# Kernel optimization log

Measured on AMD Instinct MI355X. Metric: run time of the kernel, lower is better.

Reference implementation:

```python
import jax, jax.numpy as jnp
import numpy as np

PATCH = 3  # patch_size=3 -> 3x3 displacement window, kernel_size=1, stride=1, dilation_patch=1

def _corr_level(feat1, feat2, channels):
    # spatial_correlation_sample(feat1, feat2, kernel_size=1, patch_size=3,
    #                            stride=1, padding=0, dilation_patch=1)
    # out[b, pi, pj, y, x] = sum_c feat1[b,c,y,x] * feat2[b,c, y+pi-1, x+pj-1]
    b, c, h, w = feat1.shape
    f2p = jnp.pad(feat2, ((0, 0), (0, 0), (1, 1), (1, 1)))  # zero pad displacements
    planes = []
    for di in range(PATCH):
        for dj in range(PATCH):
            planes.append(jnp.sum(feat1 * f2p[:, :, di:di + h, dj:dj + w], axis=1))
    corr = jnp.stack(planes, axis=1)  # [b, 9, h, w] == view(b, ph*pw, h, w)
    return jax.nn.leaky_relu(corr / channels, negative_slope=0.01)


def setup_inputs() -> dict:
    key = jax.random.key(0)
    chans = [512, 1024, 512, 256, 256, 256]
    sizes = [64, 32, 16, 8, 4, 2]
    B = 16
    ks = jax.random.split(key, 12)
    inp = {}
    for i, (c, s) in enumerate(zip(chans, sizes)):
        inp[f"x_pre{i}"] = jax.random.normal(ks[i], (B, c, s, s), dtype=jnp.float32)
        inp[f"x{i}"] = jax.random.normal(ks[6 + i], (B, c, s, s), dtype=jnp.float32)
    return inp


def reference(x_pre0, x_pre1, x_pre2, x_pre3, x_pre4, x_pre5,
              x0, x1, x2, x3, x4, x5):
    chans = [512, 1024, 512, 256, 256, 256]
    x_pre = [x_pre0, x_pre1, x_pre2, x_pre3, x_pre4, x_pre5]
    x = [x0, x1, x2, x3, x4, x5]
    # zip(x, x_pre): feat1 comes from x (current), feat2 from x_pre (previous)
    return tuple(_corr_level(f1, f2, c) for f1, f2, c in zip(x, x_pre, chans))
```

## Files before the change

kernel.cpp:

```cpp
#include <hip/hip_runtime.h>
#include <stdint.h>


struct Lv {
  const float* f1;
  const float* f2;
  float* dst;
  int C, ss, csize;
  uint32_t tiles;
  uint32_t npix;
  uint32_t blk_end;
};
struct P { Lv lv[6]; };

struct Fv {
  const float* src;
  uint32_t end;
  uint32_t cstride;
  uint32_t nchunk;
  int ss;
  float invC;
};
struct PF { Fv f[6]; uint32_t total; };

#define LOADIT(A, R0, R1, R2)                 \
  do {                                        \
    (A) = *(const float2*)f1p;                \
    (R0) = *(const float2*)(f2b + ro0);       \
    (R1) = *(const float2*)(f2b + ro1);       \
    (R2) = *(const float2*)(f2b + ro2);       \
    f1p += S2;                                \
    f2b += S2;                                \
  } while (0)

#define FMAROW(A, R, r)                                   \
  do {                                                    \
    const float pw = __shfl_up((R).y, 1);                 \
    const float nx = __shfl_down((R).x, 1);               \
    acc[r][0][0] = fmaf((A).x, pw, acc[r][0][0]);         \
    acc[r][0][1] = fmaf((A).y, (R).x, acc[r][0][1]);      \
    acc[r][1][0] = fmaf((A).x, (R).x, acc[r][1][0]);      \
    acc[r][1][1] = fmaf((A).y, (R).y, acc[r][1][1]);      \
    acc[r][2][0] = fmaf((A).x, (R).y, acc[r][2][0]);      \
    acc[r][2][1] = fmaf((A).y, nx, acc[r][2][1]);         \
  } while (0)

#define FMAIT(A, R0, R1, R2) \
  do {                       \
    FMAROW(A, R0, 0);        \
    FMAROW(A, R1, 1);        \
    FMAROW(A, R2, 2);        \
  } while (0)

__global__ __launch_bounds__(512, 6) void corr_part(P p) {
  __shared__ float red[8][9 * 128];

  const uint32_t bid = blockIdx.x;
  int l = 0;
#pragma unroll
  for (int i = 0; i < 5; ++i) l += (bid >= p.lv[i].blk_end) ? 1 : 0;
  const Lv L = p.lv[l];
  const uint32_t local = bid - (l ? p.lv[l - 1].blk_end : 0u);
  const uint32_t chunk = local / L.tiles;
  const uint32_t tile = local - chunk * L.tiles;

  const int w = (int)(threadIdx.x >> 6);
  const int lane = (int)(threadIdx.x & 63u);
  const int ss = L.ss;
  const int S = 1 << ss;
  const int S2 = 1 << (2 * ss);

  uint32_t pix0 = tile * 128u + ((uint32_t)lane << 1);
  if (pix0 >= L.npix) pix0 = L.npix - 2u;
  const uint32_t b = pix0 >> (2 * ss);
  const uint32_t yx = pix0 & (uint32_t)(S2 - 1);
  const int y = (int)(yx >> ss);
  const int x0 = (int)(yx & (uint32_t)(S - 1));
  (void)x0;

  const uint32_t c0 = chunk * (uint32_t)(8 * L.csize) + (uint32_t)(w * L.csize);
  const size_t pbase = ((size_t)(b * (uint32_t)L.C + c0)) << (2 * ss);
  const float* __restrict__ f1p = L.f1 + pbase + yx;
  const float* __restrict__ f2b = L.f2 + pbase;

  int yy0 = y - 1;
  yy0 = yy0 < 0 ? 0 : yy0;
  int yy2 = y + 1;
  yy2 = yy2 > S - 1 ? S - 1 : yy2;
  const int xb = (int)(yx & (uint32_t)(S - 1));
  const int ro0 = yy0 * S + xb;
  const int ro1 = y * S + xb;
  const int ro2 = yy2 * S + xb;

  float acc[3][3][2];
#pragma unroll
  for (int r = 0; r < 3; ++r)
#pragma unroll
    for (int d = 0; d < 3; ++d)
#pragma unroll
      for (int e = 0; e < 2; ++e) acc[r][d][e] = 0.f;

  const int n = L.csize;
  float2 a0, u0, v0, w0;
  float2 a1, u1, v1, w1;
  LOADIT(a0, u0, v0, w0);
#pragma unroll 1
  for (int j = 0; j + 2 < n; j += 2) {
    LOADIT(a1, u1, v1, w1);
    FMAIT(a0, u0, v0, w0);
    LOADIT(a0, u0, v0, w0);
    FMAIT(a1, u1, v1, w1);
  }
  LOADIT(a1, u1, v1, w1);
  FMAIT(a0, u0, v0, w0);
  FMAIT(a1, u1, v1, w1);

#pragma unroll
  for (int r = 0; r < 3; ++r)
#pragma unroll
    for (int d = 0; d < 3; ++d) {
      const int t = r * 3 + d;
      *(float2*)&red[w][t * 128 + lane * 2] = make_float2(acc[r][d][0], acc[r][d][1]);
    }

  __syncthreads();

  float* dbase = L.dst + (size_t)chunk * 9u * (size_t)L.npix;
  for (int idx = (int)threadIdx.x; idx < 9 * 128; idx += 512) {
    float s = 0.f;
#pragma unroll
    for (int ww = 0; ww < 8; ++ww) s += red[ww][idx];
    const int t = idx >> 7;
    const int pl = idx & 127;
    const uint32_t px = tile * 128u + (uint32_t)pl;
    if (px < L.npix) {
      const uint32_t bb = px >> (2 * ss);
      const uint32_t pyx = px & (uint32_t)(S2 - 1);
      dbase[(((size_t)(bb * 9u + (uint32_t)t)) << (2 * ss)) + pyx] = s;
    }
  }
}

__global__ __launch_bounds__(256) void corr_fin(PF p, float* __restrict__ out) {
  const uint32_t e = blockIdx.x * 256u + threadIdx.x;
  if (e >= p.total) return;
  int l = 0;
#pragma unroll
  for (int i = 0; i < 5; ++i) l += (e >= p.f[i].end) ? 1 : 0;
  const Fv F = p.f[l];
  const int ss = F.ss;
  const int S = 1 << ss;
  const int S2 = 1 << (2 * ss);
  const uint32_t local = e - (F.end - F.cstride);
  const uint32_t bt = local >> (2 * ss);
  const uint32_t yx = local & (uint32_t)(S2 - 1);
  const uint32_t t = bt % 9u;
  const int y = (int)(yx >> ss);
  const int x = (int)(yx & (uint32_t)(S - 1));
  const int di = (int)t / 3 - 1;
  const int dj = (int)t % 3 - 1;
  const int qy = y + di;
  const int qx = x + dj;

  float s = 0.f;
  for (uint32_t k = 0; k < F.nchunk; ++k) s += F.src[(size_t)k * F.cstride + local];

  float v = 0.f;
  if ((qy >= 0) & (qy < S) & (qx >= 0) & (qx < S)) {
    v = s * F.invC;
    v = v >= 0.f ? v : 0.01f * v;
  }
  out[e] = v;
}

extern "C" void kernel_launch(void* const* d_in, const int* in_sizes, int n_in,
                              void* d_out, int out_size, void* d_ws, size_t ws_size,
                              hipStream_t stream) {
  static const int CH[6] = {512, 1024, 512, 256, 256, 256};
  static const int LG[6] = {6, 5, 4, 3, 2, 1};
  int NCK[6] = {2, 4, 2, 1, 1, 1};

  const bool interleaved = (n_in >= 2) && (in_sizes[0] == in_sizes[1]);

  uint32_t npixs[6], ooff[6], oacc = 0;
  for (int i = 0; i < 6; ++i) {
    npixs[i] = 16u << (2 * LG[i]);
    ooff[i] = oacc;
    oacc += 9u * npixs[i];
  }

  size_t wneed = 0;
  for (int i = 0; i < 6; ++i) wneed += (size_t)NCK[i] * 9u * npixs[i];
  wneed *= sizeof(float);
  const bool fb = (d_ws == nullptr) || (ws_size < wneed);
  if (fb)
    for (int i = 0; i < 6; ++i) NCK[i] = 1;

  P p;
  PF pf;
  float* ws = (float*)d_ws;
  float* out = (float*)d_out;
  uint32_t bend = 0;
  size_t woff = 0;
  for (int i = 0; i < 6; ++i) {
    const uint32_t tiles = (npixs[i] + 127u) / 128u;
    Lv& L = p.lv[i];
    L.f1 = (const float*)d_in[interleaved ? (2 * i + 1) : (6 + i)];
    L.f2 = (const float*)d_in[interleaved ? (2 * i) : i];
    L.dst = fb ? (out + ooff[i]) : (ws + woff);
    L.C = CH[i];
    L.ss = LG[i];
    L.csize = CH[i] / (8 * NCK[i]);
    L.tiles = tiles;
    L.npix = npixs[i];
    bend += tiles * (uint32_t)NCK[i];
    L.blk_end = bend;

    Fv& F = pf.f[i];
    F.src = L.dst;
    F.end = ooff[i] + 9u * npixs[i];
    F.cstride = 9u * npixs[i];
    F.nchunk = (uint32_t)NCK[i];
    F.ss = LG[i];
    F.invC = 1.0f / (float)CH[i];
    woff += (size_t)NCK[i] * 9u * npixs[i];
  }
  pf.total = oacc;

  corr_part<<<bend, 512, 0, stream>>>(p);
  corr_fin<<<(oacc + 255u) / 256u, 256, 0, stream>>>(pf, out);
}
```

Baseline: 399.9 us.

## Compute 2x2 pixel quads per thread and double channel split chunks

Each thread now computes a 2x2 output quad instead of a 1x2 pair, loading four f2 rows for two f1 rows so the middle rows are shared between the two output rows. This cuts f2 loads per output and raises arithmetic intensity, at the cost of doubling the accumulators to 36 floats, which adds register pressure. With half as many pixel tiles per level, the channel split is doubled when the workspace allows, to keep the block count up. The LDS reduction is done in two halves with extra barriers.

```diff
diff --git a/kernel.cpp b/kernel.cpp
--- a/kernel.cpp
+++ b/kernel.cpp
@@ -8,7 +8,7 @@
   float* dst;
   int C, ss, csize;
   uint32_t tiles;
-  uint32_t npix;
+  uint32_t nquads;
   uint32_t blk_end;
 };
 struct P { Lv lv[6]; };
@@ -23,33 +23,39 @@
 };
 struct PF { Fv f[6]; uint32_t total; };
 
-#define LOADIT(A, R0, R1, R2)                 \
-  do {                                        \
-    (A) = *(const float2*)f1p;                \
-    (R0) = *(const float2*)(f2b + ro0);       \
-    (R1) = *(const float2*)(f2b + ro1);       \
-    (R2) = *(const float2*)(f2b + ro2);       \
-    f1p += S2;                                \
-    f2b += S2;                                \
+#define LOADIT(A0, A1, R0, R1, R2, R3)   \
+  do {                                   \
+    (A0) = *(const float2*)(f1b + o1);   \
+    (A1) = *(const float2*)(f1b + o2);   \
+    (R0) = *(const float2*)(f2b + o0);   \
+    (R1) = *(const float2*)(f2b + o1);   \
+    (R2) = *(const float2*)(f2b + o2);   \
+    (R3) = *(const float2*)(f2b + o3);   \
+    f1b += S2;                           \
+    f2b += S2;                           \
   } while (0)
 
-#define FMAROW(A, R, r)                                   \
-  do {                                                    \
-    const float pw = __shfl_up((R).y, 1);                 \
-    const float nx = __shfl_down((R).x, 1);               \
-    acc[r][0][0] = fmaf((A).x, pw, acc[r][0][0]);         \
-    acc[r][0][1] = fmaf((A).y, (R).x, acc[r][0][1]);      \
-    acc[r][1][0] = fmaf((A).x, (R).x, acc[r][1][0]);      \
-    acc[r][1][1] = fmaf((A).y, (R).y, acc[r][1][1]);      \
-    acc[r][2][0] = fmaf((A).x, (R).y, acc[r][2][0]);      \
-    acc[r][2][1] = fmaf((A).y, nx, acc[r][2][1]);         \
-  } while (0)
-
-#define FMAIT(A, R0, R1, R2) \
-  do {                       \
-    FMAROW(A, R0, 0);        \
-    FMAROW(A, R1, 1);        \
-    FMAROW(A, R2, 2);        \
+#define FMAIT(A0, A1, R0, R1, R2, R3)                              \
+  do {                                                             \
+    const float2 rr_[4] = {R0, R1, R2, R3};                        \
+    float pw_[4], nx_[4];                                          \
+    _Pragma("unroll") for (int m_ = 0; m_ < 4; ++m_) {             \
+      pw_[m_] = __shfl_up(rr_[m_].y, 1);                           \
+      nx_[m_] = __shfl_down(rr_[m_].x, 1);                         \
+    }                                                              \
+    _Pragma("unroll") for (int r_ = 0; r_ < 2; ++r_) {             \
+      const float2 a_ = r_ ? (A1) : (A0);                          \
+      _Pragma("unroll") for (int d_ = 0; d_ < 3; ++d_) {           \
+        const float2 R_ = rr_[r_ + d_];                            \
+        const float p_ = pw_[r_ + d_], n_ = nx_[r_ + d_];          \
+        acc[r_][d_][0][0] = fmaf(a_.x, p_, acc[r_][d_][0][0]);     \
+        acc[r_][d_][0][1] = fmaf(a_.y, R_.x, acc[r_][d_][0][1]);   \
+        acc[r_][d_][1][0] = fmaf(a_.x, R_.x, acc[r_][d_][1][0]);   \
+        acc[r_][d_][1][1] = fmaf(a_.y, R_.y, acc[r_][d_][1][1]);   \
+        acc[r_][d_][2][0] = fmaf(a_.x, R_.y, acc[r_][d_][2][0]);   \
+        acc[r_][d_][2][1] = fmaf(a_.y, n_, acc[r_][d_][2][1]);     \
+      }                                                            \
+    }                                                              \
   } while (0)
 
 __global__ __launch_bounds__(512, 6) void corr_part(P p) {
@@ -69,75 +75,89 @@
   const int ss = L.ss;
   const int S = 1 << ss;
   const int S2 = 1 << (2 * ss);
-
-  uint32_t pix0 = tile * 128u + ((uint32_t)lane << 1);
-  if (pix0 >= L.npix) pix0 = L.npix - 2u;
-  const uint32_t b = pix0 >> (2 * ss);
-  const uint32_t yx = pix0 & (uint32_t)(S2 - 1);
-  const int y = (int)(yx >> ss);
-  const int x0 = (int)(yx & (uint32_t)(S - 1));
-  (void)x0;
+  const uint32_t qpiM = (1u << (2 * ss - 2)) - 1u;
+  const uint32_t qrwM = (1u << (ss - 1)) - 1u;
+
+  uint32_t g = tile * 64u + (uint32_t)lane;
+  if (g >= L.nquads) g = L.nquads - 1u;
+  const uint32_t b = g >> (2 * ss - 2);
+  const uint32_t qyx = g & qpiM;
+  const int y0 = (int)((qyx >> (ss - 1)) << 1);
 
   const uint32_t c0 = chunk * (uint32_t)(8 * L.csize) + (uint32_t)(w * L.csize);
   const size_t pbase = ((size_t)(b * (uint32_t)L.C + c0)) << (2 * ss);
-  const float* __restrict__ f1p = L.f1 + pbase + yx;
+  const float* __restrict__ f1b = L.f1 + pbase;
   const float* __restrict__ f2b = L.f2 + pbase;
 
-  int yy0 = y - 1;
-  yy0 = yy0 < 0 ? 0 : yy0;
-  int yy2 = y + 1;
-  yy2 = yy2 > S - 1 ? S - 1 : yy2;
-  const int xb = (int)(yx & (uint32_t)(S - 1));
-  const int ro0 = yy0 * S + xb;
-  const int ro1 = y * S + xb;
-  const int ro2 = yy2 * S + xb;
-
-  float acc[3][3][2];
-#pragma unroll
-  for (int r = 0; r < 3; ++r)
+  const int ym = (y0 - 1) < 0 ? 0 : (y0 - 1);
+  const int yp = (y0 + 2) > (S - 1) ? (S - 1) : (y0 + 2);
+  const int xb = (int)((qyx & qrwM) << 1);
+  const int o0 = ym * S + xb;
+  const int o1 = y0 * S + xb;
+  const int o2 = o1 + S;
+  const int o3 = yp * S + xb;
+
+  float acc[2][3][3][2];
+#pragma unroll
+  for (int r = 0; r < 2; ++r)
 #pragma unroll
     for (int d = 0; d < 3; ++d)
 #pragma unroll
-      for (int e = 0; e < 2; ++e) acc[r][d][e] = 0.f;
+      for (int dd = 0; dd < 3; ++dd) {
+        acc[r][d][dd][0] = 0.f;
+        acc[r][d][dd][1] = 0.f;
+      }
 
   const int n = L.csize;
-  float2 a0, u0, v0, w0;
-  float2 a1, u1, v1, w1;
-  LOADIT(a0, u0, v0, w0);
+  float2 a00, a01, u0, v0, w0, z0;
+  float2 a10, a11, u1, v1, w1, z1;
+  LOADIT(a00, a01, u0, v0, w0, z0);
 #pragma unroll 1
   for (int j = 0; j + 2 < n; j += 2) {
-    LOADIT(a1, u1, v1, w1);
-    FMAIT(a0, u0, v0, w0);
-    LOADIT(a0, u0, v0, w0);
-    FMAIT(a1, u1, v1, w1);
-  }
-  LOADIT(a1, u1, v1, w1);
-  FMAIT(a0, u0, v0, w0);
-  FMAIT(a1, u1, v1, w1);
-
-#pragma unroll
-  for (int r = 0; r < 3; ++r)
-#pragma unroll
-    for (int d = 0; d < 3; ++d) {
-      const int t = r * 3 + d;
-      *(float2*)&red[w][t * 128 + lane * 2] = make_float2(acc[r][d][0], acc[r][d][1]);
+    LOADIT(a10, a11, u1, v1, w1, z1);
+    FMAIT(a00, a01, u0, v0, w0, z0);
+    LOADIT(a00, a01, u0, v0, w0, z0);
+    FMAIT(a10, a11, u1, v1, w1, z1);
+  }
+  LOADIT(a10, a11, u1, v1, w1, z1);
+  FMAIT(a00, a01, u0, v0, w0, z0);
+  FMAIT(a10, a11, u1, v1, w1, z1);
+
+  float* dbase = L.dst + (size_t)chunk * 9u * ((size_t)L.nquads << 2);
+#pragma unroll
+  for (int h = 0; h < 2; ++h) {
+    if ((lane >> 5) == h) {
+      const int q = lane & 31;
+#pragma unroll
+      for (int r = 0; r < 2; ++r)
+#pragma unroll
+        for (int d = 0; d < 3; ++d)
+#pragma unroll
+          for (int dd = 0; dd < 3; ++dd) {
+            const int t = d * 3 + dd;
+            *(float2*)&red[w][t * 128 + q * 4 + r * 2] =
+                make_float2(acc[r][d][dd][0], acc[r][d][dd][1]);
+          }
     }
-
-  __syncthreads();
-
-  float* dbase = L.dst + (size_t)chunk * 9u * (size_t)L.npix;
-  for (int idx = (int)threadIdx.x; idx < 9 * 128; idx += 512) {
-    float s = 0.f;
-#pragma unroll
-    for (int ww = 0; ww < 8; ++ww) s += red[ww][idx];
-    const int t = idx >> 7;
-    const int pl = idx & 127;
-    const uint32_t px = tile * 128u + (uint32_t)pl;
-    if (px < L.npix) {
-      const uint32_t bb = px >> (2 * ss);
-      const uint32_t pyx = px & (uint32_t)(S2 - 1);
-      dbase[(((size_t)(bb * 9u + (uint32_t)t)) << (2 * ss)) + pyx] = s;
+    __syncthreads();
+    for (int idx = (int)threadIdx.x; idx < 9 * 128; idx += 512) {
+      float s = 0.f;
+#pragma unroll
+      for (int ww = 0; ww < 8; ++ww) s += red[ww][idx];
+      const int t = idx >> 7;
+      const int pl = idx & 127;
+      const uint32_t g2 = tile * 64u + (uint32_t)(h * 32) + (uint32_t)(pl >> 2);
+      if (g2 < L.nquads) {
+        const int k = pl & 3;
+        const uint32_t b2 = g2 >> (2 * ss - 2);
+        const uint32_t qyx2 = g2 & qpiM;
+        const int yy = (int)((qyx2 >> (ss - 1)) << 1) + (k >> 1);
+        const int xx = (int)((qyx2 & qrwM) << 1) + (k & 1);
+        dbase[(((size_t)(b2 * 9u + (uint32_t)t)) << (2 * ss)) +
+              (uint32_t)(yy * S + xx)] = s;
+      }
     }
+    __syncthreads();
   }
 }
 
@@ -178,7 +198,7 @@
                               hipStream_t stream) {
   static const int CH[6] = {512, 1024, 512, 256, 256, 256};
   static const int LG[6] = {6, 5, 4, 3, 2, 1};
-  int NCK[6] = {2, 4, 2, 1, 1, 1};
+  static const int BASE[6] = {2, 4, 2, 1, 1, 1};
 
   const bool interleaved = (n_in >= 2) && (in_sizes[0] == in_sizes[1]);
 
@@ -189,12 +209,17 @@
     oacc += 9u * npixs[i];
   }
 
-  size_t wneed = 0;
-  for (int i = 0; i < 6; ++i) wneed += (size_t)NCK[i] * 9u * npixs[i];
-  wneed *= sizeof(float);
-  const bool fb = (d_ws == nullptr) || (ws_size < wneed);
-  if (fb)
-    for (int i = 0; i < 6; ++i) NCK[i] = 1;
+  size_t need1 = 0;
+  for (int i = 0; i < 6; ++i) need1 += (size_t)BASE[i] * 9u * npixs[i];
+  need1 *= sizeof(float);
+  const size_t need2 = need1 * 2u;
+  int mode;
+  if (d_ws && ws_size >= need2) mode = 2;
+  else if (d_ws && ws_size >= need1) mode = 1;
+  else mode = 0;
+
+  int NCK[6];
+  for (int i = 0; i < 6; ++i) NCK[i] = (mode == 0) ? 1 : BASE[i] * mode;
 
   P p;
   PF pf;
@@ -203,16 +228,17 @@
   uint32_t bend = 0;
   size_t woff = 0;
   for (int i = 0; i < 6; ++i) {
-    const uint32_t tiles = (npixs[i] + 127u) / 128u;
+    const uint32_t nquads = npixs[i] >> 2;
+    const uint32_t tiles = (nquads + 63u) / 64u;
     Lv& L = p.lv[i];
     L.f1 = (const float*)d_in[interleaved ? (2 * i + 1) : (6 + i)];
     L.f2 = (const float*)d_in[interleaved ? (2 * i) : i];
-    L.dst = fb ? (out + ooff[i]) : (ws + woff);
+    L.dst = (mode == 0) ? (out + ooff[i]) : (ws + woff);
     L.C = CH[i];
     L.ss = LG[i];
     L.csize = CH[i] / (8 * NCK[i]);
     L.tiles = tiles;
-    L.npix = npixs[i];
+    L.nquads = nquads;
     bend += tiles * (uint32_t)NCK[i];
     L.blk_end = bend;
 
```

After: 429.3 us. +7.4%, slower.
